# Performance work log

Measured on AMD Instinct MI355X. Metric: run time of the kernel, lower is better.

## Reference

```python
import jax, jax.numpy as jnp
import numpy as np

N = 8192
IN_F = 512
OUT_F = 128
NEG_BIG = -9.0e15


def setup_inputs() -> dict:
    key = jax.random.key(0)
    k_x, k_adj, k_w, k_a1, k_a2 = jax.random.split(key, 5)
    X = jax.random.normal(k_x, (N, IN_F), dtype=jnp.float32)
    adj = jax.random.randint(k_adj, (N, N), 0, 2, dtype=jnp.int32)
    # xavier_uniform with gain=1.414
    gain = 1.414
    lim_w = gain * np.sqrt(6.0 / (IN_F + OUT_F))
    W = jax.random.uniform(k_w, (IN_F, OUT_F), minval=-lim_w, maxval=lim_w, dtype=jnp.float32)
    lim_a = gain * np.sqrt(6.0 / (OUT_F + 1))
    a_1 = jax.random.uniform(k_a1, (OUT_F, 1), minval=-lim_a, maxval=lim_a, dtype=jnp.float32)
    a_2 = jax.random.uniform(k_a2, (OUT_F, 1), minval=-lim_a, maxval=lim_a, dtype=jnp.float32)
    return {"X": X, "adj": adj, "W": W, "a_1": a_1, "a_2": a_2}


def reference(X, adj, W, a_1, a_2):
    h = X @ W                         # [N, out]
    Wh1 = h @ a_1                     # [N, 1]
    Wh2 = h @ a_2                     # [N, 1]
    alpha = Wh1 + Wh2.T               # [N, N] broadcast score sum
    s = jax.nn.sigmoid(alpha)
    masked = jnp.where(adj > 0, s, jnp.float32(NEG_BIG))
    attn = jax.nn.softmax(masked, axis=1)  # dropout p=0.0 -> identity
    return attn @ h                   # [N, out]
```

## Files before the change

kernel.cpp:

```cpp
#include <hip/hip_runtime.h>
#include <hip/hip_bf16.h>

#define N_NODES 8192
#define IN_F 512
#define OUT_F 128
#define NSTRIPE 8
#define KT_PER 32
#define NWORDS (N_NODES / 32)
#define LOG2E 1.4426950408889634f

typedef unsigned short u16;
typedef unsigned int u32;
typedef short s16x8 __attribute__((ext_vector_type(8)));
typedef float f32x4 __attribute__((ext_vector_type(4)));
typedef u32 u32x4 __attribute__((ext_vector_type(4)));

__device__ __forceinline__ u16 f2bf(float f) {
    union { float f; unsigned u; } x; x.f = f;
    unsigned r = x.u + 0x7FFFu + ((x.u >> 16) & 1u);
    return (u16)(r >> 16);
}

__device__ __forceinline__ u32 packbf2(float a, float b) {
    __hip_bfloat162 h = __float22bfloat162_rn(make_float2(a, b));
    u32 u; __builtin_memcpy(&u, &h, 4);
    return u;
}

__device__ __forceinline__ float edge_p(float wh1, float w2, int keep) {
    float alpha = wh1 + w2;
    float e = exp2f(-LOG2E * alpha);
    float s = __builtin_amdgcn_rcpf(1.0f + e);
    float p = exp2f(LOG2E * s);
    return keep ? p : 0.0f;
}

__global__ void repack_W(const float* __restrict__ W, u16* __restrict__ W_frag) {
    int tid = blockIdx.x * 256 + threadIdx.x;
    int j = tid & 7;
    int lane = (tid >> 3) & 63;
    int nt = (tid >> 9) & 7;
    int kt = tid >> 12;
    int k = kt * 32 + (lane >> 4) * 8 + j;
    int n = nt * 16 + (lane & 15);
    W_frag[tid] = f2bf(W[k * OUT_F + n]);
}

__global__ void compute_Wa(const float* __restrict__ W, const float* __restrict__ a1,
                           const float* __restrict__ a2,
                           float* __restrict__ Wa1, float* __restrict__ Wa2) {
    int k = blockIdx.x * 256 + threadIdx.x;
    if (k >= IN_F) return;
    float s1 = 0.f, s2 = 0.f;
    #pragma unroll 8
    for (int n = 0; n < OUT_F; n++) {
        float w = W[k * OUT_F + n];
        s1 += w * a1[n];
        s2 += w * a2[n];
    }
    Wa1[k] = s1; Wa2[k] = s2;
}

__global__ __launch_bounds__(256)
void pack_adj(const int* __restrict__ adj, u32* __restrict__ Pk) {
    int gid = blockIdx.x * 256 + threadIdx.x;
    const int* src = adj + (size_t)gid * 32;
    u32 b = 0;
    #pragma unroll
    for (int t = 0; t < 8; t++) {
        int4 v = *(const int4*)(src + t * 4);
        b |= (u32)(v.x > 0) << (t * 4 + 0);
        b |= (u32)(v.y > 0) << (t * 4 + 1);
        b |= (u32)(v.z > 0) << (t * 4 + 2);
        b |= (u32)(v.w > 0) << (t * 4 + 3);
    }
    Pk[gid] = b;
}

__global__ __launch_bounds__(256)
void gemm_h(const float* __restrict__ X, const u16* __restrict__ W_frag,
            const float* __restrict__ Wa1, const float* __restrict__ Wa2,
            float* __restrict__ Wh1, float* __restrict__ Wh2,
            u16* __restrict__ h_frag) {
    int tid = threadIdx.x;
    int wave = tid >> 6;
    int lane = tid & 63;
    int quad = lane >> 4;
    int lid = lane & 15;
    int rbase = blockIdx.x * 16;
    const float* xrow = X + (size_t)(rbase + lid) * IN_F;
    const s16x8* Wf = (const s16x8*)W_frag;
    f32x4 acc0 = {}, acc1 = {};
    float p1 = 0.f, p2 = 0.f;
    int nt0 = wave * 2;

    int k0p = quad * 8;
    float4 X0 = *(const float4*)(xrow + k0p);
    float4 X1 = *(const float4*)(xrow + k0p + 4);
    s16x8 B0 = Wf[nt0 * 64 + lane];
    s16x8 B1 = Wf[(nt0 + 1) * 64 + lane];
    float4 A0 = {}, A1 = {}, C0 = {}, C1 = {};
    if (wave == 0) {
        A0 = *(const float4*)(Wa1 + k0p); A1 = *(const float4*)(Wa1 + k0p + 4);
        C0 = *(const float4*)(Wa2 + k0p); C1 = *(const float4*)(Wa2 + k0p + 4);
    }

    #pragma unroll 1
    for (int kt = 0; kt < 16; kt++) {
        float4 x0 = X0, x1 = X1;
        s16x8 b0 = B0, b1 = B1;
        float4 wa = A0, wb = A1, wc = C0, wd = C1;
        int ktn = (kt + 1 < 16) ? kt + 1 : kt;
        int k0n = ktn * 32 + quad * 8;
        X0 = *(const float4*)(xrow + k0n);
        X1 = *(const float4*)(xrow + k0n + 4);
        B0 = Wf[(ktn * 8 + nt0) * 64 + lane];
        B1 = Wf[(ktn * 8 + nt0 + 1) * 64 + lane];
        if (wave == 0) {
            A0 = *(const float4*)(Wa1 + k0n); A1 = *(const float4*)(Wa1 + k0n + 4);
            C0 = *(const float4*)(Wa2 + k0n); C1 = *(const float4*)(Wa2 + k0n + 4);
        }

        u32x4 uv;
        uv.x = packbf2(x0.x, x0.y); uv.y = packbf2(x0.z, x0.w);
        uv.z = packbf2(x1.x, x1.y); uv.w = packbf2(x1.z, x1.w);
        s16x8 a = __builtin_bit_cast(s16x8, uv);
        if (wave == 0) {
            p1 += x0.x*wa.x + x0.y*wa.y + x0.z*wa.z + x0.w*wa.w
                + x1.x*wb.x + x1.y*wb.y + x1.z*wb.z + x1.w*wb.w;
            p2 += x0.x*wc.x + x0.y*wc.y + x0.z*wc.z + x0.w*wc.w
                + x1.x*wd.x + x1.y*wd.y + x1.z*wd.z + x1.w*wd.w;
        }
        acc0 = __builtin_amdgcn_mfma_f32_16x16x32_bf16(a, b0, acc0, 0, 0, 0);
        acc1 = __builtin_amdgcn_mfma_f32_16x16x32_bf16(a, b1, acc1, 0, 0, 0);
    }

    #pragma unroll
    for (int reg = 0; reg < 4; reg++) {
        int row = rbase + quad * 4 + reg;
        int ktile = row >> 5, kl = row & 31;
        int lane2 = (kl >> 3) * 16 + lid, j2 = kl & 7;
        h_frag[(size_t)((ktile * 8 + nt0) * 64 + lane2) * 8 + j2] = f2bf(acc0[reg]);
        h_frag[(size_t)((ktile * 8 + nt0 + 1) * 64 + lane2) * 8 + j2] = f2bf(acc1[reg]);
    }
    if (wave == 0) {
        p1 += __shfl_xor(p1, 16, 64); p1 += __shfl_xor(p1, 32, 64);
        p2 += __shfl_xor(p2, 16, 64); p2 += __shfl_xor(p2, 32, 64);
        if (lane < 16) { Wh1[rbase + lid] = p1; Wh2[rbase + lid] = p2; }
    }
}

__global__ __launch_bounds__(512)
void attn_fused(const u32* __restrict__ Pk, const float* __restrict__ Wh1,
                const float* __restrict__ Wh2, const u16* __restrict__ h_frag,
                float* __restrict__ out) {
    __shared__ f32x4 red[NSTRIPE][16][64];
    __shared__ float rsum_lds[NSTRIPE][32];
    float* Wh2_lds = (float*)&red[0][0][0];

    int tid = threadIdx.x;
    int wave = tid >> 6;
    int lane = tid & 63;
    int quad = lane >> 4;
    int lid = lane & 15;
    int rbase = blockIdx.x * 32;
    int r0 = rbase + lid, r1 = r0 + 16;

    {
        const float4* s = (const float4*)Wh2;
        float4* d = (float4*)Wh2_lds;
        #pragma unroll
        for (int i = 0; i < 4; i++) d[tid + i * 512] = s[tid + i * 512];
    }
    float wh10 = Wh1[r0], wh11 = Wh1[r1];
    __syncthreads();

    f32x4 acc0[8] = {}, acc1[8] = {};
    float ps0 = 0.f, ps1 = 0.f;
    const s16x8* Hf = (const s16x8*)h_frag;
    const u32* prow0 = Pk + (size_t)r0 * NWORDS;
    const u32* prow1 = Pk + (size_t)r1 * NWORDS;
    const int kt0 = wave * KT_PER;

    u32x4 PA = *(const u32x4*)(prow0 + kt0);
    u32x4 PB = *(const u32x4*)(prow1 + kt0);
    s16x8 hb0[8], hb1[8];
    #pragma unroll
    for (int nt = 0; nt < 8; nt++) hb0[nt] = Hf[(kt0 * 8 + nt) * 64 + lane];

    auto step = [&](int i, u32 pw0, u32 pw1, s16x8 (&cur)[8], s16x8 (&nxt)[8]) {
        int kt = kt0 + i;
        int ktn = (i + 1 < KT_PER) ? kt + 1 : kt;
        #pragma unroll
        for (int nt = 0; nt < 8; nt++) nxt[nt] = Hf[(ktn * 8 + nt) * 64 + lane];

        int k0 = kt * 32 + quad * 8;
        float4 w20 = *(const float4*)(Wh2_lds + k0);
        float4 w21 = *(const float4*)(Wh2_lds + k0 + 4);
        u32 w0 = pw0 >> (quad * 8);
        u32 w1 = pw1 >> (quad * 8);

        float e0 = edge_p(wh10, w20.x, (w0 >> 0) & 1);
        float e1 = edge_p(wh10, w20.y, (w0 >> 1) & 1);
        float e2 = edge_p(wh10, w20.z, (w0 >> 2) & 1);
        float e3 = edge_p(wh10, w20.w, (w0 >> 3) & 1);
        float e4 = edge_p(wh10, w21.x, (w0 >> 4) & 1);
        float e5 = edge_p(wh10, w21.y, (w0 >> 5) & 1);
        float e6 = edge_p(wh10, w21.z, (w0 >> 6) & 1);
        float e7 = edge_p(wh10, w21.w, (w0 >> 7) & 1);
        ps0 += ((e0 + e1) + (e2 + e3)) + ((e4 + e5) + (e6 + e7));
        u32x4 uv0;
        uv0.x = packbf2(e0, e1); uv0.y = packbf2(e2, e3);
        uv0.z = packbf2(e4, e5); uv0.w = packbf2(e6, e7);

        float f0 = edge_p(wh11, w20.x, (w1 >> 0) & 1);
        float f1 = edge_p(wh11, w20.y, (w1 >> 1) & 1);
        float f2 = edge_p(wh11, w20.z, (w1 >> 2) & 1);
        float f3 = edge_p(wh11, w20.w, (w1 >> 3) & 1);
        float f4 = edge_p(wh11, w21.x, (w1 >> 4) & 1);
        float f5 = edge_p(wh11, w21.y, (w1 >> 5) & 1);
        float f6 = edge_p(wh11, w21.z, (w1 >> 6) & 1);
        float f7 = edge_p(wh11, w21.w, (w1 >> 7) & 1);
        ps1 += ((f0 + f1) + (f2 + f3)) + ((f4 + f5) + (f6 + f7));
        u32x4 uv1;
        uv1.x = packbf2(f0, f1); uv1.y = packbf2(f2, f3);
        uv1.z = packbf2(f4, f5); uv1.w = packbf2(f6, f7);

        s16x8 af0 = __builtin_bit_cast(s16x8, uv0);
        s16x8 af1 = __builtin_bit_cast(s16x8, uv1);

        #pragma unroll
        for (int nt = 0; nt < 8; nt++) {
            acc0[nt] = __builtin_amdgcn_mfma_f32_16x16x32_bf16(af0, cur[nt], acc0[nt], 0, 0, 0);
            acc1[nt] = __builtin_amdgcn_mfma_f32_16x16x32_bf16(af1, cur[nt], acc1[nt], 0, 0, 0);
        }
    };

    #pragma unroll 1
    for (int g = 0; g < KT_PER / 4; g++) {
        int base = g * 4;
        u32x4 cPA = PA, cPB = PB;
        int gb = (g + 1 < KT_PER / 4) ? (kt0 + base + 4) : kt0;
        PA = *(const u32x4*)(prow0 + gb);
        PB = *(const u32x4*)(prow1 + gb);
        step(base + 0, cPA.x, cPB.x, hb0, hb1);
        step(base + 1, cPA.y, cPB.y, hb1, hb0);
        step(base + 2, cPA.z, cPB.z, hb0, hb1);
        step(base + 3, cPA.w, cPB.w, hb1, hb0);
    }

    ps0 += __shfl_xor(ps0, 16, 64); ps0 += __shfl_xor(ps0, 32, 64);
    ps1 += __shfl_xor(ps1, 16, 64); ps1 += __shfl_xor(ps1, 32, 64);
    if (lane < 16) {
        rsum_lds[wave][lane] = ps0;
        rsum_lds[wave][lane + 16] = ps1;
    }

    __syncthreads();

    #pragma unroll
    for (int nt = 0; nt < 8; nt++) {
        red[wave][nt][lane] = acc0[nt];
        red[wave][nt + 8][lane] = acc1[nt];
    }
    __syncthreads();

    #pragma unroll
    for (int half = 0; half < 2; half++) {
        int i = wave + half * 8;
        int rowoff = half * 16;
        f32x4 s = red[0][i][lane];
        #pragma unroll
        for (int p2 = 1; p2 < NSTRIPE; p2++) s += red[p2][i][lane];

        #pragma unroll
        for (int reg = 0; reg < 4; reg++) {
            int rowl = quad * 4 + reg;
            float sum = 0.f;
            #pragma unroll
            for (int p2 = 0; p2 < NSTRIPE; p2++) sum += rsum_lds[p2][rowoff + rowl];
            float r = __builtin_amdgcn_rcpf(sum);
            r = r * (2.0f - sum * r);
            out[(size_t)(rbase + rowoff + rowl) * OUT_F + wave * 16 + lid] = s[reg] * r;
        }
    }
}

extern "C" void kernel_launch(void* const* d_in, const int* in_sizes, int n_in,
                              void* d_out, int out_size, void* d_ws, size_t ws_size,
                              hipStream_t stream) {
    const float* X   = (const float*)d_in[0];
    const int*   adj = (const int*)d_in[1];
    const float* W   = (const float*)d_in[2];
    const float* a1  = (const float*)d_in[3];
    const float* a2  = (const float*)d_in[4];

    char* ws = (char*)d_ws;
    float* Wh1 = (float*)(ws);
    float* Wh2 = (float*)(ws + (32 << 10));
    float* Wa1 = (float*)(ws + (64 << 10));
    float* Wa2 = (float*)(ws + (66 << 10));
    u16* W_frag = (u16*)(ws + (128 << 10));
    u16* h_frag = (u16*)(ws + (256 << 10));
    u32* Pk     = (u32*)(ws + ((size_t)4 << 20));
    float* out = (float*)d_out;

    hipLaunchKernelGGL(repack_W, dim3(256), dim3(256), 0, stream, W, W_frag);
    hipLaunchKernelGGL(compute_Wa, dim3(2), dim3(256), 0, stream, W, a1, a2, Wa1, Wa2);
    hipLaunchKernelGGL(pack_adj, dim3(N_NODES * NWORDS / 256), dim3(256), 0, stream, adj, Pk);
    hipLaunchKernelGGL(gemm_h, dim3(512), dim3(256), 0, stream,
                       X, W_frag, Wa1, Wa2, Wh1, Wh2, h_frag);
    hipLaunchKernelGGL(attn_fused, dim3(N_NODES / 32), dim3(512), 0, stream,
                       Pk, Wh1, Wh2, h_frag, out);
}
```

Baseline: 452.3 us.

## Split attention across K into partial blocks with a finalize reduction kernel

The attention kernel now splits the key dimension across 16 blocks per 128-row tile. Each block writes unnormalized partial outputs and row sums to global memory, and a new finalize kernel adds the partials and divides by the row sum. The three setup kernels are merged into one prep launch, and gemm_h moves to 8 waves with one N-tile each. The aim is more independent blocks for occupancy and fewer launches, at the cost of a 64MB partial buffer round trip. It also drops the LDS staging of Wh2 and the double-buffered prefetch of h fragments.

```diff
diff --git a/kernel.cpp b/kernel.cpp
--- a/kernel.cpp
+++ b/kernel.cpp
@@ -4,8 +4,8 @@
 #define N_NODES 8192
 #define IN_F 512
 #define OUT_F 128
-#define NSTRIPE 8
-#define KT_PER 32
+#define KP 16
+#define KT_PER 16
 #define NWORDS (N_NODES / 32)
 #define LOG2E 1.4426950408889634f
 
@@ -35,49 +35,49 @@
     return keep ? p : 0.0f;
 }
 
-__global__ void repack_W(const float* __restrict__ W, u16* __restrict__ W_frag) {
-    int tid = blockIdx.x * 256 + threadIdx.x;
-    int j = tid & 7;
-    int lane = (tid >> 3) & 63;
-    int nt = (tid >> 9) & 7;
-    int kt = tid >> 12;
-    int k = kt * 32 + (lane >> 4) * 8 + j;
-    int n = nt * 16 + (lane & 15);
-    W_frag[tid] = f2bf(W[k * OUT_F + n]);
-}
-
-__global__ void compute_Wa(const float* __restrict__ W, const float* __restrict__ a1,
-                           const float* __restrict__ a2,
-                           float* __restrict__ Wa1, float* __restrict__ Wa2) {
-    int k = blockIdx.x * 256 + threadIdx.x;
-    if (k >= IN_F) return;
-    float s1 = 0.f, s2 = 0.f;
-    #pragma unroll 8
-    for (int n = 0; n < OUT_F; n++) {
-        float w = W[k * OUT_F + n];
-        s1 += w * a1[n];
-        s2 += w * a2[n];
-    }
-    Wa1[k] = s1; Wa2[k] = s2;
-}
-
 __global__ __launch_bounds__(256)
-void pack_adj(const int* __restrict__ adj, u32* __restrict__ Pk) {
-    int gid = blockIdx.x * 256 + threadIdx.x;
-    const int* src = adj + (size_t)gid * 32;
-    u32 b = 0;
-    #pragma unroll
-    for (int t = 0; t < 8; t++) {
-        int4 v = *(const int4*)(src + t * 4);
-        b |= (u32)(v.x > 0) << (t * 4 + 0);
-        b |= (u32)(v.y > 0) << (t * 4 + 1);
-        b |= (u32)(v.z > 0) << (t * 4 + 2);
-        b |= (u32)(v.w > 0) << (t * 4 + 3);
-    }
-    Pk[gid] = b;
-}
-
-__global__ __launch_bounds__(256)
+void prep(const int* __restrict__ adj, const float* __restrict__ W,
+          const float* __restrict__ a1, const float* __restrict__ a2,
+          u32* __restrict__ Pk, u16* __restrict__ W_frag,
+          float* __restrict__ Wa1, float* __restrict__ Wa2) {
+    int b = blockIdx.x;
+    int tid = threadIdx.x;
+    if (b < 8192) {
+        int gid = b * 256 + tid;
+        const int* src = adj + (size_t)gid * 32;
+        u32 bits = 0;
+        #pragma unroll
+        for (int t = 0; t < 8; t++) {
+            int4 v = *(const int4*)(src + t * 4);
+            bits |= (u32)(v.x > 0) << (t * 4 + 0);
+            bits |= (u32)(v.y > 0) << (t * 4 + 1);
+            bits |= (u32)(v.z > 0) << (t * 4 + 2);
+            bits |= (u32)(v.w > 0) << (t * 4 + 3);
+        }
+        Pk[gid] = bits;
+    } else if (b < 8448) {
+        int t2 = (b - 8192) * 256 + tid;
+        int j = t2 & 7;
+        int lane = (t2 >> 3) & 63;
+        int nt = (t2 >> 9) & 7;
+        int kt = t2 >> 12;
+        int k = kt * 32 + (lane >> 4) * 8 + j;
+        int n = nt * 16 + (lane & 15);
+        W_frag[t2] = f2bf(W[k * OUT_F + n]);
+    } else {
+        int k = (b - 8448) * 256 + tid;
+        float s1 = 0.f, s2 = 0.f;
+        #pragma unroll 8
+        for (int n = 0; n < OUT_F; n++) {
+            float w = W[k * OUT_F + n];
+            s1 += w * a1[n];
+            s2 += w * a2[n];
+        }
+        Wa1[k] = s1; Wa2[k] = s2;
+    }
+}
+
+__global__ __launch_bounds__(512)
 void gemm_h(const float* __restrict__ X, const u16* __restrict__ W_frag,
             const float* __restrict__ Wa1, const float* __restrict__ Wa2,
             float* __restrict__ Wh1, float* __restrict__ Wh2,
@@ -90,15 +90,14 @@
     int rbase = blockIdx.x * 16;
     const float* xrow = X + (size_t)(rbase + lid) * IN_F;
     const s16x8* Wf = (const s16x8*)W_frag;
-    f32x4 acc0 = {}, acc1 = {};
+    f32x4 acc = {};
     float p1 = 0.f, p2 = 0.f;
-    int nt0 = wave * 2;
+    int nt0 = wave;
 
     int k0p = quad * 8;
     float4 X0 = *(const float4*)(xrow + k0p);
     float4 X1 = *(const float4*)(xrow + k0p + 4);
     s16x8 B0 = Wf[nt0 * 64 + lane];
-    s16x8 B1 = Wf[(nt0 + 1) * 64 + lane];
     float4 A0 = {}, A1 = {}, C0 = {}, C1 = {};
     if (wave == 0) {
         A0 = *(const float4*)(Wa1 + k0p); A1 = *(const float4*)(Wa1 + k0p + 4);
@@ -108,14 +107,13 @@
     #pragma unroll 1
     for (int kt = 0; kt < 16; kt++) {
         float4 x0 = X0, x1 = X1;
-        s16x8 b0 = B0, b1 = B1;
+        s16x8 b0 = B0;
         float4 wa = A0, wb = A1, wc = C0, wd = C1;
         int ktn = (kt + 1 < 16) ? kt + 1 : kt;
         int k0n = ktn * 32 + quad * 8;
         X0 = *(const float4*)(xrow + k0n);
         X1 = *(const float4*)(xrow + k0n + 4);
         B0 = Wf[(ktn * 8 + nt0) * 64 + lane];
-        B1 = Wf[(ktn * 8 + nt0 + 1) * 64 + lane];
         if (wave == 0) {
             A0 = *(const float4*)(Wa1 + k0n); A1 = *(const float4*)(Wa1 + k0n + 4);
             C0 = *(const float4*)(Wa2 + k0n); C1 = *(const float4*)(Wa2 + k0n + 4);
@@ -131,8 +129,7 @@
             p2 += x0.x*wc.x + x0.y*wc.y + x0.z*wc.z + x0.w*wc.w
                 + x1.x*wd.x + x1.y*wd.y + x1.z*wd.z + x1.w*wd.w;
         }
-        acc0 = __builtin_amdgcn_mfma_f32_16x16x32_bf16(a, b0, acc0, 0, 0, 0);
-        acc1 = __builtin_amdgcn_mfma_f32_16x16x32_bf16(a, b1, acc1, 0, 0, 0);
+        acc = __builtin_amdgcn_mfma_f32_16x16x32_bf16(a, b0, acc, 0, 0, 0);
     }
 
     #pragma unroll
@@ -140,8 +137,7 @@
         int row = rbase + quad * 4 + reg;
         int ktile = row >> 5, kl = row & 31;
         int lane2 = (kl >> 3) * 16 + lid, j2 = kl & 7;
-        h_frag[(size_t)((ktile * 8 + nt0) * 64 + lane2) * 8 + j2] = f2bf(acc0[reg]);
-        h_frag[(size_t)((ktile * 8 + nt0 + 1) * 64 + lane2) * 8 + j2] = f2bf(acc1[reg]);
+        h_frag[(size_t)((ktile * 8 + nt0) * 64 + lane2) * 8 + j2] = f2bf(acc[reg]);
     }
     if (wave == 0) {
         p1 += __shfl_xor(p1, 16, 64); p1 += __shfl_xor(p1, 32, 64);
@@ -150,53 +146,36 @@
     }
 }
 
-__global__ __launch_bounds__(512)
-void attn_fused(const u32* __restrict__ Pk, const float* __restrict__ Wh1,
-                const float* __restrict__ Wh2, const u16* __restrict__ h_frag,
-                float* __restrict__ out) {
-    __shared__ f32x4 red[NSTRIPE][16][64];
-    __shared__ float rsum_lds[NSTRIPE][32];
-    float* Wh2_lds = (float*)&red[0][0][0];
-
+__global__ __launch_bounds__(256)
+void attn_kernel(const u32* __restrict__ Pk, const float* __restrict__ Wh1,
+                 const float* __restrict__ Wh2, const u16* __restrict__ h_frag,
+                 float* __restrict__ out_part, float* __restrict__ sum_part) {
     int tid = threadIdx.x;
     int wave = tid >> 6;
     int lane = tid & 63;
     int quad = lane >> 4;
     int lid = lane & 15;
-    int rbase = blockIdx.x * 32;
+    int rtile = blockIdx.x >> 4;
+    int kh = blockIdx.x & (KP - 1);
+    int rbase = rtile * 128 + wave * 32;
     int r0 = rbase + lid, r1 = r0 + 16;
 
-    {
-        const float4* s = (const float4*)Wh2;
-        float4* d = (float4*)Wh2_lds;
-        #pragma unroll
-        for (int i = 0; i < 4; i++) d[tid + i * 512] = s[tid + i * 512];
-    }
     float wh10 = Wh1[r0], wh11 = Wh1[r1];
-    __syncthreads();
-
     f32x4 acc0[8] = {}, acc1[8] = {};
     float ps0 = 0.f, ps1 = 0.f;
     const s16x8* Hf = (const s16x8*)h_frag;
     const u32* prow0 = Pk + (size_t)r0 * NWORDS;
     const u32* prow1 = Pk + (size_t)r1 * NWORDS;
-    const int kt0 = wave * KT_PER;
+    const int kt0 = kh * KT_PER;
 
     u32x4 PA = *(const u32x4*)(prow0 + kt0);
     u32x4 PB = *(const u32x4*)(prow1 + kt0);
-    s16x8 hb0[8], hb1[8];
-    #pragma unroll
-    for (int nt = 0; nt < 8; nt++) hb0[nt] = Hf[(kt0 * 8 + nt) * 64 + lane];
-
-    auto step = [&](int i, u32 pw0, u32 pw1, s16x8 (&cur)[8], s16x8 (&nxt)[8]) {
+
+    auto step = [&](int i, u32 pw0, u32 pw1) {
         int kt = kt0 + i;
-        int ktn = (i + 1 < KT_PER) ? kt + 1 : kt;
-        #pragma unroll
-        for (int nt = 0; nt < 8; nt++) nxt[nt] = Hf[(ktn * 8 + nt) * 64 + lane];
-
         int k0 = kt * 32 + quad * 8;
-        float4 w20 = *(const float4*)(Wh2_lds + k0);
-        float4 w21 = *(const float4*)(Wh2_lds + k0 + 4);
+        float4 w20 = *(const float4*)(Wh2 + k0);
+        float4 w21 = *(const float4*)(Wh2 + k0 + 4);
         u32 w0 = pw0 >> (quad * 8);
         u32 w1 = pw1 >> (quad * 8);
 
@@ -231,59 +210,54 @@
 
         #pragma unroll
         for (int nt = 0; nt < 8; nt++) {
-            acc0[nt] = __builtin_amdgcn_mfma_f32_16x16x32_bf16(af0, cur[nt], acc0[nt], 0, 0, 0);
-            acc1[nt] = __builtin_amdgcn_mfma_f32_16x16x32_bf16(af1, cur[nt], acc1[nt], 0, 0, 0);
+            s16x8 b = Hf[(kt * 8 + nt) * 64 + lane];
+            acc0[nt] = __builtin_amdgcn_mfma_f32_16x16x32_bf16(af0, b, acc0[nt], 0, 0, 0);
+            acc1[nt] = __builtin_amdgcn_mfma_f32_16x16x32_bf16(af1, b, acc1[nt], 0, 0, 0);
         }
     };
 
     #pragma unroll 1
     for (int g = 0; g < KT_PER / 4; g++) {
-        int base = g * 4;
         u32x4 cPA = PA, cPB = PB;
-        int gb = (g + 1 < KT_PER / 4) ? (kt0 + base + 4) : kt0;
+        int gb = kt0 + ((g + 1 < KT_PER / 4) ? (g + 1) * 4 : 0);
         PA = *(const u32x4*)(prow0 + gb);
         PB = *(const u32x4*)(prow1 + gb);
-        step(base + 0, cPA.x, cPB.x, hb0, hb1);
-        step(base + 1, cPA.y, cPB.y, hb1, hb0);
-        step(base + 2, cPA.z, cPB.z, hb0, hb1);
-        step(base + 3, cPA.w, cPB.w, hb1, hb0);
+        step(g * 4 + 0, cPA.x, cPB.x);
+        step(g * 4 + 1, cPA.y, cPB.y);
+        step(g * 4 + 2, cPA.z, cPB.z);
+        step(g * 4 + 3, cPA.w, cPB.w);
     }
 
     ps0 += __shfl_xor(ps0, 16, 64); ps0 += __shfl_xor(ps0, 32, 64);
     ps1 += __shfl_xor(ps1, 16, 64); ps1 += __shfl_xor(ps1, 32, 64);
-    if (lane < 16) {
-        rsum_lds[wave][lane] = ps0;
-        rsum_lds[wave][lane + 16] = ps1;
-    }
-
-    __syncthreads();
+    if (quad == 0) {
+        sum_part[(size_t)kh * N_NODES + r0] = ps0;
+        sum_part[(size_t)kh * N_NODES + r1] = ps1;
+    }
 
     #pragma unroll
     for (int nt = 0; nt < 8; nt++) {
-        red[wave][nt][lane] = acc0[nt];
-        red[wave][nt + 8][lane] = acc1[nt];
-    }
-    __syncthreads();
-
-    #pragma unroll
-    for (int half = 0; half < 2; half++) {
-        int i = wave + half * 8;
-        int rowoff = half * 16;
-        f32x4 s = red[0][i][lane];
-        #pragma unroll
-        for (int p2 = 1; p2 < NSTRIPE; p2++) s += red[p2][i][lane];
-
         #pragma unroll
         for (int reg = 0; reg < 4; reg++) {
-            int rowl = quad * 4 + reg;
-            float sum = 0.f;
-            #pragma unroll
-            for (int p2 = 0; p2 < NSTRIPE; p2++) sum += rsum_lds[p2][rowoff + rowl];
-            float r = __builtin_amdgcn_rcpf(sum);
-            r = r * (2.0f - sum * r);
-            out[(size_t)(rbase + rowoff + rowl) * OUT_F + wave * 16 + lid] = s[reg] * r;
-        }
-    }
+            int row0 = rbase + quad * 4 + reg;
+            int col = nt * 16 + lid;
+            out_part[((size_t)kh * N_NODES + row0) * OUT_F + col] = acc0[nt][reg];
+            out_part[((size_t)kh * N_NODES + row0 + 16) * OUT_F + col] = acc1[nt][reg];
+        }
+    }
+}
+
+__global__ void finalize(const float* __restrict__ out_part,
+                         const float* __restrict__ sum_part,
+                         float* __restrict__ out) {
+    int gid = blockIdx.x * 256 + threadIdx.x;
+    int i = gid >> 7;
+    float s = 0.f, v = 0.f;
+    for (int kh = 0; kh < KP; kh++) {
+        s += sum_part[(size_t)kh * N_NODES + i];
+        v += out_part[(size_t)kh * N_NODES * OUT_F + gid];
+    }
+    out[gid] = v / s;
 }
 
 extern "C" void kernel_launch(void* const* d_in, const int* in_sizes, int n_in,
@@ -303,13 +277,16 @@
     u16* W_frag = (u16*)(ws + (128 << 10));
     u16* h_frag = (u16*)(ws + (256 << 10));
     u32* Pk     = (u32*)(ws + ((size_t)4 << 20));
+    float* out_part = (float*)(ws + ((size_t)16 << 20));
+    float* sum_part = (float*)(ws + ((size_t)80 << 20));
     float* out = (float*)d_out;
 
-    hipLaunchKernelGGL(repack_W, dim3(256), dim3(256), 0, stream, W, W_frag);
-    hipLaunchKernelGGL(compute_Wa, dim3(2), dim3(256), 0, stream, W, a1, a2, Wa1, Wa2);
-    hipLaunchKernelGGL(pack_adj, dim3(N_NODES * NWORDS / 256), dim3(256), 0, stream, adj, Pk);
-    hipLaunchKernelGGL(gemm_h, dim3(512), dim3(256), 0, stream,
+    hipLaunchKernelGGL(prep, dim3(8450), dim3(256), 0, stream,
+                       adj, W, a1, a2, Pk, W_frag, Wa1, Wa2);
+    hipLaunchKernelGGL(gemm_h, dim3(512), dim3(512), 0, stream,
                        X, W_frag, Wa1, Wa2, Wh1, Wh2, h_frag);
-    hipLaunchKernelGGL(attn_fused, dim3(N_NODES / 32), dim3(512), 0, stream,
-                       Pk, Wh1, Wh2, h_frag, out);
-}
+    hipLaunchKernelGGL(attn_kernel, dim3(64 * KP), dim3(256), 0, stream,
+                       Pk, Wh1, Wh2, h_frag, out_part, sum_part);
+    hipLaunchKernelGGL(finalize, dim3((N_NODES * OUT_F) / 256), dim3(256), 0, stream,
+                       out_part, sum_part, out);
+}
```

Result: slower. 461.9 us (+2.1%).
